# Optimization experiments

Hardware: AMD Instinct MI355X
Metric: run time of the kernel (lower is better)

## Reference

```python
import jax, jax.numpy as jnp
import numpy as np

BN_EPS = 1e-5


def gcn_conv(x, src, dst, n, W, b):
    # PyG GCNConv: h = x @ W; add self-loops; symmetric deg^{-1/2} norm; scatter-add; + bias
    h = x @ W
    sl = jnp.arange(n, dtype=src.dtype)
    src_f = jnp.concatenate([src, sl])
    dst_f = jnp.concatenate([dst, sl])
    deg = jax.ops.segment_sum(jnp.ones_like(dst_f, dtype=h.dtype), dst_f, num_segments=n)
    dis = jnp.where(deg > 0, jax.lax.rsqrt(jnp.maximum(deg, 1.0)), 0.0)
    norm = dis[src_f] * dis[dst_f]                       # [E+N]
    msg = h[src_f] * norm[:, None]                       # gather + scale
    out = jax.ops.segment_sum(msg, dst_f, num_segments=n)  # scatter-add
    return out + b


def batchnorm(x, g, b):
    # training-mode BatchNorm1d (batch statistics), deterministic
    mu = jnp.mean(x, axis=0)
    var = jnp.mean((x - mu) ** 2, axis=0)
    return g * (x - mu) * jax.lax.rsqrt(var + BN_EPS) + b


def setup_inputs() -> dict:
    key = jax.random.key(0)
    ks = jax.random.split(key, 12)
    N, E, F_IN, D, M, G = 40000, 640000, 128, 128, 256, 2000
    x = jax.random.normal(ks[0], (N, F_IN), dtype=jnp.float32)
    edge_index = jax.random.randint(ks[1], (2, E), 0, N, dtype=jnp.int64)
    batch = jnp.sort(jax.random.randint(ks[2], (N,), 0, G, dtype=jnp.int64))
    s = lambda fi: 1.0 / np.sqrt(fi)
    W1 = jax.random.normal(ks[3], (F_IN, D), dtype=jnp.float32) * s(F_IN)
    b1 = jnp.zeros((D,), jnp.float32)
    W2 = jax.random.normal(ks[4], (D, D), dtype=jnp.float32) * s(D)
    b2 = jnp.zeros((D,), jnp.float32)
    bn1_g = jnp.ones((D,), jnp.float32); bn1_b = jnp.zeros((D,), jnp.float32)
    bn2_g = jnp.ones((D,), jnp.float32); bn2_b = jnp.zeros((D,), jnp.float32)
    fc1_w = jax.random.normal(ks[5], (D, M), dtype=jnp.float32) * s(D)
    fc1_b = jnp.zeros((M,), jnp.float32)
    fc2_w = jax.random.normal(ks[6], (M, M), dtype=jnp.float32) * s(M)
    fc2_b = jnp.zeros((M,), jnp.float32)
    fc3_w = jax.random.normal(ks[7], (M, 1), dtype=jnp.float32) * s(M)
    fc3_b = jnp.zeros((1,), jnp.float32)
    return dict(x=x, edge_index=edge_index, batch=batch, num_graphs=G,
                W1=W1, b1=b1, W2=W2, b2=b2,
                bn1_g=bn1_g, bn1_b=bn1_b, bn2_g=bn2_g, bn2_b=bn2_b,
                fc1_w=fc1_w, fc1_b=fc1_b, fc2_w=fc2_w, fc2_b=fc2_b,
                fc3_w=fc3_w, fc3_b=fc3_b)


def reference(x, edge_index, batch, num_graphs, W1, b1, W2, b2,
              bn1_g, bn1_b, bn2_g, bn2_b,
              fc1_w, fc1_b, fc2_w, fc2_b, fc3_w, fc3_b):
    n = x.shape[0]
    src, dst = edge_index[0], edge_index[1]
    h = gcn_conv(x, src, dst, n, W1, b1)
    h = jax.nn.relu(batchnorm(h, bn1_g, bn1_b))
    h = gcn_conv(h, src, dst, n, W2, b2)
    h = jax.nn.relu(batchnorm(h, bn2_g, bn2_b))
    g = jax.ops.segment_sum(h, batch, num_segments=num_graphs)  # scatter_sum pooling [G, D]
    g = jax.nn.relu(g @ fc1_w + fc1_b)   # dropout is identity in eval
    g = jax.nn.relu(g @ fc2_w + fc2_b)
    return g @ fc3_w + fc3_b             # [G, 1]
```

## Files before the change

kernel.cpp:

```cpp
#include <hip/hip_runtime.h>

#define NN 40000
#define NE 640000
#define DF 128
#define NG 2000
#define NCH 157
#define FILLB 625
#define GEMM_BLKS 313

typedef unsigned int u32;
typedef __attribute__((ext_vector_type(8))) short short8;
typedef __attribute__((ext_vector_type(4))) float floatx4;

__device__ inline float2 bf2_to_f2(u32 u) {
    return make_float2(__uint_as_float(u << 16), __uint_as_float(u & 0xffff0000u));
}
__device__ inline u32 f_to_bf(float f) {
    u32 u = __float_as_uint(f);
    return (u + 0x7fffu + ((u >> 16) & 1u)) >> 16;
}
__device__ inline u32 pack_bf2(float a, float b) {
    return f_to_bf(a) | (f_to_bf(b) << 16);
}
__device__ inline float bf_to_f(short s) {
    return __uint_as_float(((u32)(unsigned short)s) << 16);
}

template<bool BF16IN, bool FUSE_BN, bool WT_F32>
__device__ __forceinline__ void gemm_core(const void* __restrict__ Xv, const void* __restrict__ wsrc,
                                          u32* __restrict__ outb, const float* __restrict__ slots,
                                          const float* __restrict__ gam, const float* __restrict__ bet, int bid) {
    __shared__ unsigned short uni[128 * 136];
    __shared__ float sc[128], sh[128];
    unsigned short* wlds = uni;
    unsigned short* clds = uni;
    int tid = threadIdx.x;
    int row0 = bid * 128;

    if (FUSE_BN) {
        if (tid < 128) {
            float s = 0.f, q = 0.f;
            for (int k = 0; k < 64; k++) {
                s += slots[k * 256 + tid];
                q += slots[k * 256 + 128 + tid];
            }
            const float inv_n = 1.0f / (float)NN;
            float mu = s * inv_n;
            float va = fmaf(-mu, mu, q * inv_n);
            float a = gam[tid] * rsqrtf(va + 1e-5f);
            sc[tid] = a;
            sh[tid] = fmaf(-mu, a, bet[tid]);
        }
    }
    if (WT_F32) {
        const float* W = (const float*)wsrc;
        for (int i = tid; i < 16384; i += 256) {
            int k = i >> 7, c = i & 127;
            wlds[c * 136 + k] = (unsigned short)f_to_bf(W[i]);
        }
    } else {
        const unsigned short* wt = (const unsigned short*)wsrc;
        for (int i = tid; i < 2048; i += 256) {
            int c = i >> 4, s = i & 15;
            *(uint4*)&wlds[c * 136 + s * 8] = ((const uint4*)wt)[i];
        }
    }
    __syncthreads();

    int lane = tid & 63;
    int wave = tid >> 6;
    int qr = lane >> 4;
    int rl = lane & 15;
    int rA0 = row0 + wave * 32 + rl;
    int rA1 = rA0 + 16;
    int rA0c = rA0 < NN ? rA0 : NN - 1;
    int rA1c = rA1 < NN ? rA1 : NN - 1;

    floatx4 acc[2][8];
#pragma unroll
    for (int a = 0; a < 2; a++)
#pragma unroll
        for (int b = 0; b < 8; b++) acc[a][b] = (floatx4){0.f, 0.f, 0.f, 0.f};

#pragma unroll
    for (int kb = 0; kb < 4; kb++) {
        int k0 = kb * 32 + qr * 8;
        short8 a0, a1;
        if (!BF16IN) {
            const float* p0 = (const float*)Xv + (size_t)rA0c * DF + k0;
            const float* p1 = (const float*)Xv + (size_t)rA1c * DF + k0;
            float4 u0 = *(const float4*)p0, u1 = *(const float4*)(p0 + 4);
            float4 v0 = *(const float4*)p1, v1 = *(const float4*)(p1 + 4);
            float fa[8] = {u0.x, u0.y, u0.z, u0.w, u1.x, u1.y, u1.z, u1.w};
            float fb[8] = {v0.x, v0.y, v0.z, v0.w, v1.x, v1.y, v1.z, v1.w};
#pragma unroll
            for (int j = 0; j < 8; j++) { a0[j] = (short)f_to_bf(fa[j]); a1[j] = (short)f_to_bf(fb[j]); }
        } else {
            a0 = *(const short8*)((const u32*)Xv + (size_t)rA0c * 64 + (k0 >> 1));
            a1 = *(const short8*)((const u32*)Xv + (size_t)rA1c * 64 + (k0 >> 1));
            if (FUSE_BN) {
                float4 s0 = *(const float4*)&sc[k0], s1 = *(const float4*)&sc[k0 + 4];
                float4 h0 = *(const float4*)&sh[k0], h1 = *(const float4*)&sh[k0 + 4];
                float ss[8] = {s0.x, s0.y, s0.z, s0.w, s1.x, s1.y, s1.z, s1.w};
                float hh[8] = {h0.x, h0.y, h0.z, h0.w, h1.x, h1.y, h1.z, h1.w};
#pragma unroll
                for (int j = 0; j < 8; j++) {
                    float f0 = fmaxf(fmaf(bf_to_f(a0[j]), ss[j], hh[j]), 0.f);
                    float f1 = fmaxf(fmaf(bf_to_f(a1[j]), ss[j], hh[j]), 0.f);
                    a0[j] = (short)f_to_bf(f0);
                    a1[j] = (short)f_to_bf(f1);
                }
            }
        }
#pragma unroll
        for (int ct = 0; ct < 8; ct++) {
            short8 bfr = *(const short8*)&wlds[(ct * 16 + rl) * 136 + k0];
            acc[0][ct] = __builtin_amdgcn_mfma_f32_16x16x32_bf16(a0, bfr, acc[0][ct], 0, 0, 0);
            acc[1][ct] = __builtin_amdgcn_mfma_f32_16x16x32_bf16(a1, bfr, acc[1][ct], 0, 0, 0);
        }
    }
    __syncthreads();
#pragma unroll
    for (int rt = 0; rt < 2; rt++)
#pragma unroll
        for (int ct = 0; ct < 8; ct++)
#pragma unroll
            for (int r = 0; r < 4; r++) {
                int lr = wave * 32 + rt * 16 + qr * 4 + r;
                int c = ct * 16 + rl;
                clds[lr * 136 + c] = (unsigned short)f_to_bf(acc[rt][ct][r]);
            }
    __syncthreads();
    for (int i = tid; i < 2048; i += 256) {
        int lr = i >> 4, s = i & 15;
        int grow = row0 + lr;
        if (grow < NN) {
            uint4 v = *(const uint4*)&clds[lr * 136 + s * 8];
            ((uint4*)(outb + (size_t)grow * 64))[s] = v;
        }
    }
}

__global__ __launch_bounds__(256, 4) void k_countgemm(const int* __restrict__ dst, int* __restrict__ deg,
                                                      int* __restrict__ rank,
                                                      const float* __restrict__ W1, const float* __restrict__ W2,
                                                      unsigned short* __restrict__ wt2,
                                                      const float* __restrict__ X, u32* __restrict__ outb) {
    int bid = blockIdx.x;
    if (bid < FILLB) {
        int e0 = bid * 1024 + threadIdx.x;
        int d0 = dst[e0], d1 = dst[e0 + 256], d2 = dst[e0 + 512], d3 = dst[e0 + 768];
        int r0 = atomicAdd(&deg[d0], 1);
        int r1 = atomicAdd(&deg[d1], 1);
        int r2 = atomicAdd(&deg[d2], 1);
        int r3 = atomicAdd(&deg[d3], 1);
        rank[e0] = r0;
        rank[e0 + 256] = r1;
        rank[e0 + 512] = r2;
        rank[e0 + 768] = r3;
        return;
    }
    if (bid == FILLB) {
        for (int i = threadIdx.x; i < 128 * 128; i += 256) {
            int k = i >> 7, c = i & 127;
            wt2[c * 128 + k] = (unsigned short)f_to_bf(W2[i]);
        }
        return;
    }
    gemm_core<false, false, true>(X, W1, outb, nullptr, nullptr, nullptr, bid - FILLB - 1);
}

__global__ __launch_bounds__(256) void k_scan(const int* __restrict__ deg,
                                              int* __restrict__ row_ptr, float* __restrict__ dis) {
    __shared__ int red[256];
    __shared__ int ls[256];
    int tid = threadIdx.x;
    int blk = blockIdx.x;
    int limit = blk * 256;
    int partial = 0;
    for (int i = tid; i < limit; i += 256) partial += deg[i];
    red[tid] = partial;
    int i = limit + tid;
    int d = (i < NN) ? deg[i] : 0;
    ls[tid] = d;
    __syncthreads();
#pragma unroll
    for (int off = 128; off > 0; off >>= 1) {
        if (tid < off) red[tid] += red[tid + off];
        __syncthreads();
    }
    int base = red[0];
#pragma unroll
    for (int off = 1; off < 256; off <<= 1) {
        int t = (tid >= off) ? ls[tid - off] : 0;
        __syncthreads();
        ls[tid] += t;
        __syncthreads();
    }
    if (i < NN) {
        int r = base + ls[tid] - d;
        row_ptr[i] = r;
        dis[i] = rsqrtf((float)(d + 1));
    }
    if (blk == NCH - 1 && tid == 0) row_ptr[NN] = NE;
}

__global__ __launch_bounds__(256) void k_fill(const int* __restrict__ src, const int* __restrict__ dst,
                                              const int* __restrict__ rank, const int* __restrict__ row_ptr,
                                              int* __restrict__ col) {
    int e0 = blockIdx.x * 1024 + threadIdx.x;
    int d0 = dst[e0], d1 = dst[e0 + 256], d2 = dst[e0 + 512], d3 = dst[e0 + 768];
    int s0 = src[e0], s1 = src[e0 + 256], s2 = src[e0 + 512], s3 = src[e0 + 768];
    int r0 = rank[e0], r1 = rank[e0 + 256], r2 = rank[e0 + 512], r3 = rank[e0 + 768];
    col[row_ptr[d0] + r0] = s0;
    col[row_ptr[d1] + r1] = s1;
    col[row_ptr[d2] + r2] = s2;
    col[row_ptr[d3] + r3] = s3;
}

__global__ __launch_bounds__(256, 4) void k_gemm2(const u32* __restrict__ Hb, const unsigned short* __restrict__ wt2,
                                                  u32* __restrict__ outb, const float* __restrict__ slots,
                                                  const float* __restrict__ gam, const float* __restrict__ bet) {
    gemm_core<true, true, false>(Hb, wt2, outb, slots, gam, bet, blockIdx.x);
}

__global__ __launch_bounds__(256) void k_gather(const u32* __restrict__ Hb, const int* __restrict__ row_ptr,
                                                const int* __restrict__ col, const float* __restrict__ dis,
                                                const float* __restrict__ bias, u32* __restrict__ outb,
                                                float* __restrict__ slots) {
    __shared__ float sred[4][128];
    __shared__ float qred[4][128];
    int t = threadIdx.x & 63;
    int wv = threadIdx.x >> 6;
    int node = blockIdx.x * 4 + wv;
    float di = dis[node];
    float2 acc;
    {
        float2 a = bf2_to_f2(Hb[(size_t)node * 64 + t]);
        float s = di * di;
        acc = make_float2(a.x * s, a.y * s);
    }
    int lo = row_ptr[node], hi = row_ptr[node + 1];
    for (int base = lo; base < hi; base += 64) {
        int m = hi - base; if (m > 64) m = 64;
        int sidx = 0; float sw = 0.f;
        if (t < m) { sidx = col[base + t]; sw = di * dis[sidx]; }
        int j = 0;
        for (; j + 8 <= m; j += 8) {
            int s0 = __shfl(sidx, j),     s1 = __shfl(sidx, j + 1);
            int s2 = __shfl(sidx, j + 2), s3 = __shfl(sidx, j + 3);
            int s4 = __shfl(sidx, j + 4), s5 = __shfl(sidx, j + 5);
            int s6 = __shfl(sidx, j + 6), s7 = __shfl(sidx, j + 7);
            float w0 = __shfl(sw, j),     w1 = __shfl(sw, j + 1);
            float w2 = __shfl(sw, j + 2), w3 = __shfl(sw, j + 3);
            float w4 = __shfl(sw, j + 4), w5 = __shfl(sw, j + 5);
            float w6 = __shfl(sw, j + 6), w7 = __shfl(sw, j + 7);
            u32 u0 = Hb[(size_t)s0 * 64 + t], u1 = Hb[(size_t)s1 * 64 + t];
            u32 u2 = Hb[(size_t)s2 * 64 + t], u3 = Hb[(size_t)s3 * 64 + t];
            u32 u4 = Hb[(size_t)s4 * 64 + t], u5 = Hb[(size_t)s5 * 64 + t];
            u32 u6 = Hb[(size_t)s6 * 64 + t], u7 = Hb[(size_t)s7 * 64 + t];
            float2 h0 = bf2_to_f2(u0), h1 = bf2_to_f2(u1), h2 = bf2_to_f2(u2), h3 = bf2_to_f2(u3);
            float2 h4 = bf2_to_f2(u4), h5 = bf2_to_f2(u5), h6 = bf2_to_f2(u6), h7 = bf2_to_f2(u7);
            acc.x = fmaf(h3.x, w3, fmaf(h2.x, w2, fmaf(h1.x, w1, fmaf(h0.x, w0, acc.x))));
            acc.y = fmaf(h3.y, w3, fmaf(h2.y, w2, fmaf(h1.y, w1, fmaf(h0.y, w0, acc.y))));
            acc.x = fmaf(h7.x, w7, fmaf(h6.x, w6, fmaf(h5.x, w5, fmaf(h4.x, w4, acc.x))));
            acc.y = fmaf(h7.y, w7, fmaf(h6.y, w6, fmaf(h5.y, w5, fmaf(h4.y, w4, acc.y))));
        }
        for (; j < m; j++) {
            int s0 = __shfl(sidx, j); float w0 = __shfl(sw, j);
            float2 h0 = bf2_to_f2(Hb[(size_t)s0 * 64 + t]);
            acc.x = fmaf(h0.x, w0, acc.x);
            acc.y = fmaf(h0.y, w0, acc.y);
        }
    }
    float2 b = ((const float2*)bias)[t];
    acc.x += b.x; acc.y += b.y;
    outb[(size_t)node * 64 + t] = pack_bf2(acc.x, acc.y);
    sred[wv][2 * t] = acc.x;     sred[wv][2 * t + 1] = acc.y;
    qred[wv][2 * t] = acc.x * acc.x; qred[wv][2 * t + 1] = acc.y * acc.y;
    __syncthreads();
    int tid = threadIdx.x;
    if (tid < 128) {
        float s = sred[0][tid] + sred[1][tid] + sred[2][tid] + sred[3][tid];
        float q = qred[0][tid] + qred[1][tid] + qred[2][tid] + qred[3][tid];
        int slot = blockIdx.x & 63;
        atomicAdd(&slots[slot * 256 + tid], s);
        atomicAdd(&slots[slot * 256 + 128 + tid], q);
    }
}

__global__ __launch_bounds__(256) void k_poolfc(const u32* __restrict__ Hb, const int* __restrict__ batch,
                                                const float* __restrict__ slots,
                                                const float* __restrict__ gam, const float* __restrict__ bet,
                                                const float* __restrict__ fc1w, const float* __restrict__ fc1b,
                                                const float* __restrict__ fc2w, const float* __restrict__ fc2b,
                                                const float* __restrict__ fc3w, const float* __restrict__ fc3b,
                                                float* __restrict__ out) {
    __shared__ float sc[128], sh[128];
    __shared__ float pooled[4][128];
    __shared__ float g1[4][256];
    __shared__ float g2[4][256];
    __shared__ int bnds[5];
    int tid = threadIdx.x;
    int gbase = blockIdx.x * 4;
    if (tid < 128) {
        float s = 0.f, q = 0.f;
        for (int k = 0; k < 64; k++) {
            s += slots[k * 256 + tid];
            q += slots[k * 256 + 128 + tid];
        }
        const float inv_n = 1.0f / (float)NN;
        float mu = s * inv_n;
        float va = fmaf(-mu, mu, q * inv_n);
        float a = gam[tid] * rsqrtf(va + 1e-5f);
        sc[tid] = a;
        sh[tid] = fmaf(-mu, a, bet[tid]);
    } else if (tid < 133) {
        int target = gbase + (tid - 128);
        int a = 0, b = NN;
        while (a < b) { int m = (a + b) >> 1; if (batch[m] < target) a = m + 1; else b = m; }
        bnds[tid - 128] = a;
    }
    __syncthreads();
    {
        int g = tid >> 6, p = tid & 63;
        int lo = bnds[g], hi = bnds[g + 1];
        float a0 = 0.f, a1 = 0.f;
        float sc0 = sc[2 * p], sh0 = sh[2 * p], sc1 = sc[2 * p + 1], sh1 = sh[2 * p + 1];
        for (int i = lo; i < hi; i++) {
            float2 v = bf2_to_f2(Hb[(size_t)i * 64 + p]);
            a0 += fmaxf(fmaf(v.x, sc0, sh0), 0.f);
            a1 += fmaxf(fmaf(v.y, sc1, sh1), 0.f);
        }
        pooled[g][2 * p] = a0;
        pooled[g][2 * p + 1] = a1;
    }
    __syncthreads();
    {
        float x0 = 0.f, x1 = 0.f, x2 = 0.f, x3 = 0.f;
        for (int k = 0; k < 128; k++) {
            float wv = fc1w[k * 256 + tid];
            x0 = fmaf(pooled[0][k], wv, x0);
            x1 = fmaf(pooled[1][k], wv, x1);
            x2 = fmaf(pooled[2][k], wv, x2);
            x3 = fmaf(pooled[3][k], wv, x3);
        }
        float bb = fc1b[tid];
        g1[0][tid] = fmaxf(x0 + bb, 0.f);
        g1[1][tid] = fmaxf(x1 + bb, 0.f);
        g1[2][tid] = fmaxf(x2 + bb, 0.f);
        g1[3][tid] = fmaxf(x3 + bb, 0.f);
    }
    __syncthreads();
    {
        float x0 = 0.f, x1 = 0.f, x2 = 0.f, x3 = 0.f;
        for (int k = 0; k < 256; k++) {
            float wv = fc2w[k * 256 + tid];
            x0 = fmaf(g1[0][k], wv, x0);
            x1 = fmaf(g1[1][k], wv, x1);
            x2 = fmaf(g1[2][k], wv, x2);
            x3 = fmaf(g1[3][k], wv, x3);
        }
        float bb = fc2b[tid];
        g2[0][tid] = fmaxf(x0 + bb, 0.f);
        g2[1][tid] = fmaxf(x1 + bb, 0.f);
        g2[2][tid] = fmaxf(x2 + bb, 0.f);
        g2[3][tid] = fmaxf(x3 + bb, 0.f);
    }
    __syncthreads();
    {
        int lane = tid & 63, wv = tid >> 6;
        float s = fmaf(g2[wv][lane], fc3w[lane],
                  fmaf(g2[wv][64 + lane], fc3w[64 + lane],
                  fmaf(g2[wv][128 + lane], fc3w[128 + lane],
                       g2[wv][192 + lane] * fc3w[192 + lane])));
        for (int off = 32; off > 0; off >>= 1) s += __shfl_down(s, off);
        if (lane == 0) out[gbase + wv] = s + fc3b[0];
    }
}

extern "C" void kernel_launch(void* const* d_in, const int* in_sizes, int n_in,
                              void* d_out, int out_size, void* d_ws, size_t ws_size,
                              hipStream_t stream) {
    const float* x    = (const float*)d_in[0];
    const int*   ei   = (const int*)d_in[1];
    const int*   batch= (const int*)d_in[2];
    const float* W1   = (const float*)d_in[4];
    const float* b1   = (const float*)d_in[5];
    const float* W2   = (const float*)d_in[6];
    const float* b2   = (const float*)d_in[7];
    const float* bn1g = (const float*)d_in[8];
    const float* bn1b = (const float*)d_in[9];
    const float* bn2g = (const float*)d_in[10];
    const float* bn2b = (const float*)d_in[11];
    const float* fc1w = (const float*)d_in[12];
    const float* fc1b = (const float*)d_in[13];
    const float* fc2w = (const float*)d_in[14];
    const float* fc2b = (const float*)d_in[15];
    const float* fc3w = (const float*)d_in[16];
    const float* fc3b = (const float*)d_in[17];
    const int* src = ei;
    const int* dst = ei + NE;
    float* outp = (float*)d_out;

    char* w = (char*)d_ws;
    size_t o = 0;
    auto alloc = [&](size_t bytes) -> char* {
        char* p = w + o;
        o = (o + bytes + 255) & ~(size_t)255;
        return p;
    };
    int*   deg     = (int*)alloc((size_t)NN * 4);
    float* slotsA  = (float*)alloc(64 * 256 * 4);
    float* slotsB  = (float*)alloc(64 * 256 * 4);
    char*  zend    = w + o;
    int*   row_ptr = (int*)alloc((size_t)(NN + 1) * 4);
    int*   rank    = (int*)alloc((size_t)NE * 4);
    int*   col     = (int*)alloc((size_t)NE * 4);
    float* dis     = (float*)alloc((size_t)NN * 4);
    unsigned short* wt2 = (unsigned short*)alloc(128 * 128 * 2);
    u32*   bufA    = (u32*)alloc((size_t)NN * 64 * 4);
    u32*   bufB    = (u32*)alloc((size_t)NN * 64 * 4);

    hipMemsetAsync(deg, 0, (size_t)(zend - (char*)deg), stream);

    k_countgemm<<<FILLB + 1 + GEMM_BLKS, 256, 0, stream>>>(dst, deg, rank, W1, W2, wt2, x, bufA);
    k_scan<<<NCH, 256, 0, stream>>>(deg, row_ptr, dis);
    k_fill<<<FILLB, 256, 0, stream>>>(src, dst, rank, row_ptr, col);
    k_gather<<<NN / 4, 256, 0, stream>>>(bufA, row_ptr, col, dis, b1, bufB, slotsA);
    k_gemm2<<<GEMM_BLKS, 256, 0, stream>>>(bufB, wt2, bufA, slotsA, bn1g, bn1b);
    k_gather<<<NN / 4, 256, 0, stream>>>(bufA, row_ptr, col, dis, b2, bufB, slotsB);
    k_poolfc<<<NG / 4, 256, 0, stream>>>(bufB, batch, slotsB, bn2g, bn2b,
                                         fc1w, fc1b, fc2w, fc2b, fc3w, fc3b, outp);
}
```

Measured before the change: 276.2 us.

## Build CSR with per-block LDS degree counting and fused scan-fill

Replaces the global-atomic degree count with 157 blocks that each scan the full dst array and count edges for their own 256-node window using shared-memory atomics. The scan and fill kernels are merged into one that keeps row pointers in LDS, and the memset is replaced by zeroing blocks inside the first kernel. This removes global atomic contention, one kernel launch and a memset. In exchange every block reads all 640K dst entries, about 157x redundant reads (mostly L2 hits), and rank and col writes become scattered.

```diff
diff --git a/kernel.cpp b/kernel.cpp
--- a/kernel.cpp
+++ b/kernel.cpp
@@ -5,7 +5,6 @@
 #define DF 128
 #define NG 2000
 #define NCH 157
-#define FILLB 625
 #define GEMM_BLKS 313
 
 typedef unsigned int u32;
@@ -142,45 +141,62 @@
 }
 
 __global__ __launch_bounds__(256, 4) void k_countgemm(const int* __restrict__ dst, int* __restrict__ deg,
-                                                      int* __restrict__ rank,
+                                                      int* __restrict__ rank, float* __restrict__ slots0,
                                                       const float* __restrict__ W1, const float* __restrict__ W2,
                                                       unsigned short* __restrict__ wt2,
                                                       const float* __restrict__ X, u32* __restrict__ outb) {
+    __shared__ int wdeg[256];
     int bid = blockIdx.x;
-    if (bid < FILLB) {
-        int e0 = bid * 1024 + threadIdx.x;
-        int d0 = dst[e0], d1 = dst[e0 + 256], d2 = dst[e0 + 512], d3 = dst[e0 + 768];
-        int r0 = atomicAdd(&deg[d0], 1);
-        int r1 = atomicAdd(&deg[d1], 1);
-        int r2 = atomicAdd(&deg[d2], 1);
-        int r3 = atomicAdd(&deg[d3], 1);
-        rank[e0] = r0;
-        rank[e0 + 256] = r1;
-        rank[e0 + 512] = r2;
-        rank[e0 + 768] = r3;
+    int tid = threadIdx.x;
+    if (bid < NCH) {
+        int lo = bid << 8;
+        wdeg[tid] = 0;
+        __syncthreads();
+        const int4* dst4 = (const int4*)dst;
+        for (int it = tid; it < NE / 4; it += 256) {
+            int4 d = dst4[it];
+            int e = it * 4;
+            int t0 = d.x - lo, t1 = d.y - lo, t2 = d.z - lo, t3 = d.w - lo;
+            if ((u32)t0 < 256u) rank[e]     = atomicAdd(&wdeg[t0], 1);
+            if ((u32)t1 < 256u) rank[e + 1] = atomicAdd(&wdeg[t1], 1);
+            if ((u32)t2 < 256u) rank[e + 2] = atomicAdd(&wdeg[t2], 1);
+            if ((u32)t3 < 256u) rank[e + 3] = atomicAdd(&wdeg[t3], 1);
+        }
+        __syncthreads();
+        int node = lo + tid;
+        if (node < NN) deg[node] = wdeg[tid];
         return;
     }
-    if (bid == FILLB) {
-        for (int i = threadIdx.x; i < 128 * 128; i += 256) {
+    if (bid < NCH + 2) {
+        float* s = slots0 + (bid - NCH) * 64 * 256;
+        for (int i = tid; i < 64 * 256; i += 256) s[i] = 0.f;
+        return;
+    }
+    if (bid == NCH + 2) {
+        for (int i = tid; i < 128 * 128; i += 256) {
             int k = i >> 7, c = i & 127;
             wt2[c * 128 + k] = (unsigned short)f_to_bf(W2[i]);
         }
         return;
     }
-    gemm_core<false, false, true>(X, W1, outb, nullptr, nullptr, nullptr, bid - FILLB - 1);
-}
-
-__global__ __launch_bounds__(256) void k_scan(const int* __restrict__ deg,
-                                              int* __restrict__ row_ptr, float* __restrict__ dis) {
+    gemm_core<false, false, true>(X, W1, outb, nullptr, nullptr, nullptr, bid - NCH - 3);
+}
+
+__global__ __launch_bounds__(256) void k_scanfill(const int* __restrict__ deg,
+                                                  const int* __restrict__ src, const int* __restrict__ dst,
+                                                  const int* __restrict__ rank,
+                                                  int* __restrict__ row_ptr, float* __restrict__ dis,
+                                                  int* __restrict__ col) {
     __shared__ int red[256];
     __shared__ int ls[256];
+    __shared__ int rowp[256];
     int tid = threadIdx.x;
     int blk = blockIdx.x;
-    int limit = blk * 256;
+    int lo = blk << 8;
     int partial = 0;
-    for (int i = tid; i < limit; i += 256) partial += deg[i];
+    for (int i = tid; i < lo; i += 256) partial += deg[i];
     red[tid] = partial;
-    int i = limit + tid;
+    int i = lo + tid;
     int d = (i < NN) ? deg[i] : 0;
     ls[tid] = d;
     __syncthreads();
@@ -197,25 +213,24 @@
         ls[tid] += t;
         __syncthreads();
     }
+    int r = base + ls[tid] - d;
+    rowp[tid] = r;
     if (i < NN) {
-        int r = base + ls[tid] - d;
         row_ptr[i] = r;
         dis[i] = rsqrtf((float)(d + 1));
     }
     if (blk == NCH - 1 && tid == 0) row_ptr[NN] = NE;
-}
-
-__global__ __launch_bounds__(256) void k_fill(const int* __restrict__ src, const int* __restrict__ dst,
-                                              const int* __restrict__ rank, const int* __restrict__ row_ptr,
-                                              int* __restrict__ col) {
-    int e0 = blockIdx.x * 1024 + threadIdx.x;
-    int d0 = dst[e0], d1 = dst[e0 + 256], d2 = dst[e0 + 512], d3 = dst[e0 + 768];
-    int s0 = src[e0], s1 = src[e0 + 256], s2 = src[e0 + 512], s3 = src[e0 + 768];
-    int r0 = rank[e0], r1 = rank[e0 + 256], r2 = rank[e0 + 512], r3 = rank[e0 + 768];
-    col[row_ptr[d0] + r0] = s0;
-    col[row_ptr[d1] + r1] = s1;
-    col[row_ptr[d2] + r2] = s2;
-    col[row_ptr[d3] + r3] = s3;
+    __syncthreads();
+    const int4* dst4 = (const int4*)dst;
+    for (int it = tid; it < NE / 4; it += 256) {
+        int4 dd = dst4[it];
+        int e = it * 4;
+        int t0 = dd.x - lo, t1 = dd.y - lo, t2 = dd.z - lo, t3 = dd.w - lo;
+        if ((u32)t0 < 256u) col[rowp[t0] + rank[e]]     = src[e];
+        if ((u32)t1 < 256u) col[rowp[t1] + rank[e + 1]] = src[e + 1];
+        if ((u32)t2 < 256u) col[rowp[t2] + rank[e + 2]] = src[e + 2];
+        if ((u32)t3 < 256u) col[rowp[t3] + rank[e + 3]] = src[e + 3];
+    }
 }
 
 __global__ __launch_bounds__(256, 4) void k_gemm2(const u32* __restrict__ Hb, const unsigned short* __restrict__ wt2,
@@ -411,9 +426,7 @@
         return p;
     };
     int*   deg     = (int*)alloc((size_t)NN * 4);
-    float* slotsA  = (float*)alloc(64 * 256 * 4);
-    float* slotsB  = (float*)alloc(64 * 256 * 4);
-    char*  zend    = w + o;
+    float* slots0  = (float*)alloc((size_t)2 * 64 * 256 * 4);
     int*   row_ptr = (int*)alloc((size_t)(NN + 1) * 4);
     int*   rank    = (int*)alloc((size_t)NE * 4);
     int*   col     = (int*)alloc((size_t)NE * 4);
@@ -421,12 +434,11 @@
     unsigned short* wt2 = (unsigned short*)alloc(128 * 128 * 2);
     u32*   bufA    = (u32*)alloc((size_t)NN * 64 * 4);
     u32*   bufB    = (u32*)alloc((size_t)NN * 64 * 4);
-
-    hipMemsetAsync(deg, 0, (size_t)(zend - (char*)deg), stream);
-
-    k_countgemm<<<FILLB + 1 + GEMM_BLKS, 256, 0, stream>>>(dst, deg, rank, W1, W2, wt2, x, bufA);
-    k_scan<<<NCH, 256, 0, stream>>>(deg, row_ptr, dis);
-    k_fill<<<FILLB, 256, 0, stream>>>(src, dst, rank, row_ptr, col);
+    float* slotsA  = slots0;
+    float* slotsB  = slots0 + 64 * 256;
+
+    k_countgemm<<<NCH + 3 + GEMM_BLKS, 256, 0, stream>>>(dst, deg, rank, slots0, W1, W2, wt2, x, bufA);
+    k_scanfill<<<NCH, 256, 0, stream>>>(deg, src, dst, rank, row_ptr, dis, col);
     k_gather<<<NN / 4, 256, 0, stream>>>(bufA, row_ptr, col, dis, b1, bufB, slotsA);
     k_gemm2<<<GEMM_BLKS, 256, 0, stream>>>(bufB, wt2, bufA, slotsA, bn1g, bn1b);
     k_gather<<<NN / 4, 256, 0, stream>>>(bufA, row_ptr, col, dis, b2, bufB, slotsB);
```

Result: slower. 752.6 us (+172.4%).

## Pack fp16 source norm into CSR column word and halve GEMM row tile

Applied to the files above, without the earlier changes.

The CSR fill kernel now stores each edge's source index in the low 16 bits and an fp16 copy of the source's deg^-1/2 in the high 16 bits. The gather kernel therefore decodes the edge weight from the column word instead of doing a dependent random load of dis[src] per edge. Separately, the GEMM tiles drop from 128 to 64 rows per block, doubling the block count to raise parallelism, with the row bound checks removed because 40000 divides evenly by 64. The trade-offs are fp16 precision on the normalisation factor and a hard limit of 65536 nodes from the 16-bit index.

```diff
diff --git a/kernel.cpp b/kernel.cpp
--- a/kernel.cpp
+++ b/kernel.cpp
@@ -1,4 +1,5 @@
 #include <hip/hip_runtime.h>
+#include <hip/hip_fp16.h>
 
 #define NN 40000
 #define NE 640000
@@ -6,7 +7,7 @@
 #define NG 2000
 #define NCH 157
 #define FILLB 625
-#define GEMM_BLKS 313
+#define GEMM_BLKS 625
 
 typedef unsigned int u32;
 typedef __attribute__((ext_vector_type(8))) short short8;
@@ -24,6 +25,9 @@
 }
 __device__ inline float bf_to_f(short s) {
     return __uint_as_float(((u32)(unsigned short)s) << 16);
+}
+__device__ inline float colw_to_f(int cw) {
+    return __half2float(__ushort_as_half((unsigned short)((u32)cw >> 16)));
 }
 
 template<bool BF16IN, bool FUSE_BN, bool WT_F32>
@@ -35,7 +39,7 @@
     unsigned short* wlds = uni;
     unsigned short* clds = uni;
     int tid = threadIdx.x;
-    int row0 = bid * 128;
+    int row0 = bid * 64;
 
     if (FUSE_BN) {
         if (tid < 128) {
@@ -71,33 +75,24 @@
     int wave = tid >> 6;
     int qr = lane >> 4;
     int rl = lane & 15;
-    int rA0 = row0 + wave * 32 + rl;
-    int rA1 = rA0 + 16;
-    int rA0c = rA0 < NN ? rA0 : NN - 1;
-    int rA1c = rA1 < NN ? rA1 : NN - 1;
-
-    floatx4 acc[2][8];
-#pragma unroll
-    for (int a = 0; a < 2; a++)
-#pragma unroll
-        for (int b = 0; b < 8; b++) acc[a][b] = (floatx4){0.f, 0.f, 0.f, 0.f};
+    int rA = row0 + wave * 16 + rl;
+
+    floatx4 acc[8];
+#pragma unroll
+    for (int b = 0; b < 8; b++) acc[b] = (floatx4){0.f, 0.f, 0.f, 0.f};
 
 #pragma unroll
     for (int kb = 0; kb < 4; kb++) {
         int k0 = kb * 32 + qr * 8;
-        short8 a0, a1;
+        short8 a0;
         if (!BF16IN) {
-            const float* p0 = (const float*)Xv + (size_t)rA0c * DF + k0;
-            const float* p1 = (const float*)Xv + (size_t)rA1c * DF + k0;
+            const float* p0 = (const float*)Xv + (size_t)rA * DF + k0;
             float4 u0 = *(const float4*)p0, u1 = *(const float4*)(p0 + 4);
-            float4 v0 = *(const float4*)p1, v1 = *(const float4*)(p1 + 4);
             float fa[8] = {u0.x, u0.y, u0.z, u0.w, u1.x, u1.y, u1.z, u1.w};
-            float fb[8] = {v0.x, v0.y, v0.z, v0.w, v1.x, v1.y, v1.z, v1.w};
-#pragma unroll
-            for (int j = 0; j < 8; j++) { a0[j] = (short)f_to_bf(fa[j]); a1[j] = (short)f_to_bf(fb[j]); }
+#pragma unroll
+            for (int j = 0; j < 8; j++) a0[j] = (short)f_to_bf(fa[j]);
         } else {
-            a0 = *(const short8*)((const u32*)Xv + (size_t)rA0c * 64 + (k0 >> 1));
-            a1 = *(const short8*)((const u32*)Xv + (size_t)rA1c * 64 + (k0 >> 1));
+            a0 = *(const short8*)((const u32*)Xv + (size_t)rA * 64 + (k0 >> 1));
             if (FUSE_BN) {
                 float4 s0 = *(const float4*)&sc[k0], s1 = *(const float4*)&sc[k0 + 4];
                 float4 h0 = *(const float4*)&sh[k0], h1 = *(const float4*)&sh[k0 + 4];
@@ -106,38 +101,30 @@
 #pragma unroll
                 for (int j = 0; j < 8; j++) {
                     float f0 = fmaxf(fmaf(bf_to_f(a0[j]), ss[j], hh[j]), 0.f);
-                    float f1 = fmaxf(fmaf(bf_to_f(a1[j]), ss[j], hh[j]), 0.f);
                     a0[j] = (short)f_to_bf(f0);
-                    a1[j] = (short)f_to_bf(f1);
                 }
             }
         }
 #pragma unroll
         for (int ct = 0; ct < 8; ct++) {
             short8 bfr = *(const short8*)&wlds[(ct * 16 + rl) * 136 + k0];
-            acc[0][ct] = __builtin_amdgcn_mfma_f32_16x16x32_bf16(a0, bfr, acc[0][ct], 0, 0, 0);
-            acc[1][ct] = __builtin_amdgcn_mfma_f32_16x16x32_bf16(a1, bfr, acc[1][ct], 0, 0, 0);
-        }
-    }
-    __syncthreads();
-#pragma unroll
-    for (int rt = 0; rt < 2; rt++)
-#pragma unroll
-        for (int ct = 0; ct < 8; ct++)
-#pragma unroll
-            for (int r = 0; r < 4; r++) {
-                int lr = wave * 32 + rt * 16 + qr * 4 + r;
-                int c = ct * 16 + rl;
-                clds[lr * 136 + c] = (unsigned short)f_to_bf(acc[rt][ct][r]);
-            }
-    __syncthreads();
-    for (int i = tid; i < 2048; i += 256) {
+            acc[ct] = __builtin_amdgcn_mfma_f32_16x16x32_bf16(a0, bfr, acc[ct], 0, 0, 0);
+        }
+    }
+    __syncthreads();
+#pragma unroll
+    for (int ct = 0; ct < 8; ct++)
+#pragma unroll
+        for (int r = 0; r < 4; r++) {
+            int lr = wave * 16 + qr * 4 + r;
+            int c = ct * 16 + rl;
+            clds[lr * 136 + c] = (unsigned short)f_to_bf(acc[ct][r]);
+        }
+    __syncthreads();
+    for (int i = tid; i < 1024; i += 256) {
         int lr = i >> 4, s = i & 15;
-        int grow = row0 + lr;
-        if (grow < NN) {
-            uint4 v = *(const uint4*)&clds[lr * 136 + s * 8];
-            ((uint4*)(outb + (size_t)grow * 64))[s] = v;
-        }
+        uint4 v = *(const uint4*)&clds[lr * 136 + s * 8];
+        ((uint4*)(outb + (size_t)(row0 + lr) * 64))[s] = v;
     }
 }
 
@@ -207,15 +194,19 @@
 
 __global__ __launch_bounds__(256) void k_fill(const int* __restrict__ src, const int* __restrict__ dst,
                                               const int* __restrict__ rank, const int* __restrict__ row_ptr,
-                                              int* __restrict__ col) {
+                                              const float* __restrict__ dis, u32* __restrict__ col) {
     int e0 = blockIdx.x * 1024 + threadIdx.x;
     int d0 = dst[e0], d1 = dst[e0 + 256], d2 = dst[e0 + 512], d3 = dst[e0 + 768];
     int s0 = src[e0], s1 = src[e0 + 256], s2 = src[e0 + 512], s3 = src[e0 + 768];
     int r0 = rank[e0], r1 = rank[e0 + 256], r2 = rank[e0 + 512], r3 = rank[e0 + 768];
-    col[row_ptr[d0] + r0] = s0;
-    col[row_ptr[d1] + r1] = s1;
-    col[row_ptr[d2] + r2] = s2;
-    col[row_ptr[d3] + r3] = s3;
+    u32 h0 = (u32)__half_as_ushort(__float2half(dis[s0]));
+    u32 h1 = (u32)__half_as_ushort(__float2half(dis[s1]));
+    u32 h2 = (u32)__half_as_ushort(__float2half(dis[s2]));
+    u32 h3 = (u32)__half_as_ushort(__float2half(dis[s3]));
+    col[row_ptr[d0] + r0] = (u32)s0 | (h0 << 16);
+    col[row_ptr[d1] + r1] = (u32)s1 | (h1 << 16);
+    col[row_ptr[d2] + r2] = (u32)s2 | (h2 << 16);
+    col[row_ptr[d3] + r3] = (u32)s3 | (h3 << 16);
 }
 
 __global__ __launch_bounds__(256, 4) void k_gemm2(const u32* __restrict__ Hb, const unsigned short* __restrict__ wt2,
@@ -225,7 +216,7 @@
 }
 
 __global__ __launch_bounds__(256) void k_gather(const u32* __restrict__ Hb, const int* __restrict__ row_ptr,
-                                                const int* __restrict__ col, const float* __restrict__ dis,
+                                                const u32* __restrict__ col, const float* __restrict__ dis,
                                                 const float* __restrict__ bias, u32* __restrict__ outb,
                                                 float* __restrict__ slots) {
     __shared__ float sred[4][128];
@@ -243,22 +234,22 @@
     int lo = row_ptr[node], hi = row_ptr[node + 1];
     for (int base = lo; base < hi; base += 64) {
         int m = hi - base; if (m > 64) m = 64;
-        int sidx = 0; float sw = 0.f;
-        if (t < m) { sidx = col[base + t]; sw = di * dis[sidx]; }
+        int cw = 0;
+        if (t < m) cw = (int)col[base + t];
         int j = 0;
         for (; j + 8 <= m; j += 8) {
-            int s0 = __shfl(sidx, j),     s1 = __shfl(sidx, j + 1);
-            int s2 = __shfl(sidx, j + 2), s3 = __shfl(sidx, j + 3);
-            int s4 = __shfl(sidx, j + 4), s5 = __shfl(sidx, j + 5);
-            int s6 = __shfl(sidx, j + 6), s7 = __shfl(sidx, j + 7);
-            float w0 = __shfl(sw, j),     w1 = __shfl(sw, j + 1);
-            float w2 = __shfl(sw, j + 2), w3 = __shfl(sw, j + 3);
-            float w4 = __shfl(sw, j + 4), w5 = __shfl(sw, j + 5);
-            float w6 = __shfl(sw, j + 6), w7 = __shfl(sw, j + 7);
-            u32 u0 = Hb[(size_t)s0 * 64 + t], u1 = Hb[(size_t)s1 * 64 + t];
-            u32 u2 = Hb[(size_t)s2 * 64 + t], u3 = Hb[(size_t)s3 * 64 + t];
-            u32 u4 = Hb[(size_t)s4 * 64 + t], u5 = Hb[(size_t)s5 * 64 + t];
-            u32 u6 = Hb[(size_t)s6 * 64 + t], u7 = Hb[(size_t)s7 * 64 + t];
+            int c0 = __shfl(cw, j),     c1 = __shfl(cw, j + 1);
+            int c2 = __shfl(cw, j + 2), c3 = __shfl(cw, j + 3);
+            int c4 = __shfl(cw, j + 4), c5 = __shfl(cw, j + 5);
+            int c6 = __shfl(cw, j + 6), c7 = __shfl(cw, j + 7);
+            u32 u0 = Hb[(size_t)(c0 & 0xffff) * 64 + t], u1 = Hb[(size_t)(c1 & 0xffff) * 64 + t];
+            u32 u2 = Hb[(size_t)(c2 & 0xffff) * 64 + t], u3 = Hb[(size_t)(c3 & 0xffff) * 64 + t];
+            u32 u4 = Hb[(size_t)(c4 & 0xffff) * 64 + t], u5 = Hb[(size_t)(c5 & 0xffff) * 64 + t];
+            u32 u6 = Hb[(size_t)(c6 & 0xffff) * 64 + t], u7 = Hb[(size_t)(c7 & 0xffff) * 64 + t];
+            float w0 = di * colw_to_f(c0), w1 = di * colw_to_f(c1);
+            float w2 = di * colw_to_f(c2), w3 = di * colw_to_f(c3);
+            float w4 = di * colw_to_f(c4), w5 = di * colw_to_f(c5);
+            float w6 = di * colw_to_f(c6), w7 = di * colw_to_f(c7);
             float2 h0 = bf2_to_f2(u0), h1 = bf2_to_f2(u1), h2 = bf2_to_f2(u2), h3 = bf2_to_f2(u3);
             float2 h4 = bf2_to_f2(u4), h5 = bf2_to_f2(u5), h6 = bf2_to_f2(u6), h7 = bf2_to_f2(u7);
             acc.x = fmaf(h3.x, w3, fmaf(h2.x, w2, fmaf(h1.x, w1, fmaf(h0.x, w0, acc.x))));
@@ -267,8 +258,9 @@
             acc.y = fmaf(h7.y, w7, fmaf(h6.y, w6, fmaf(h5.y, w5, fmaf(h4.y, w4, acc.y))));
         }
         for (; j < m; j++) {
-            int s0 = __shfl(sidx, j); float w0 = __shfl(sw, j);
-            float2 h0 = bf2_to_f2(Hb[(size_t)s0 * 64 + t]);
+            int c0 = __shfl(cw, j);
+            float w0 = di * colw_to_f(c0);
+            float2 h0 = bf2_to_f2(Hb[(size_t)(c0 & 0xffff) * 64 + t]);
             acc.x = fmaf(h0.x, w0, acc.x);
             acc.y = fmaf(h0.y, w0, acc.y);
         }
@@ -416,7 +408,7 @@
     char*  zend    = w + o;
     int*   row_ptr = (int*)alloc((size_t)(NN + 1) * 4);
     int*   rank    = (int*)alloc((size_t)NE * 4);
-    int*   col     = (int*)alloc((size_t)NE * 4);
+    u32*   col     = (u32*)alloc((size_t)NE * 4);
     float* dis     = (float*)alloc((size_t)NN * 4);
     unsigned short* wt2 = (unsigned short*)alloc(128 * 128 * 2);
     u32*   bufA    = (u32*)alloc((size_t)NN * 64 * 4);
@@ -426,7 +418,7 @@
 
     k_countgemm<<<FILLB + 1 + GEMM_BLKS, 256, 0, stream>>>(dst, deg, rank, W1, W2, wt2, x, bufA);
     k_scan<<<NCH, 256, 0, stream>>>(deg, row_ptr, dis);
-    k_fill<<<FILLB, 256, 0, stream>>>(src, dst, rank, row_ptr, col);
+    k_fill<<<FILLB, 256, 0, stream>>>(src, dst, rank, row_ptr, dis, col);
     k_gather<<<NN / 4, 256, 0, stream>>>(bufA, row_ptr, col, dis, b1, bufB, slotsA);
     k_gemm2<<<GEMM_BLKS, 256, 0, stream>>>(bufB, wt2, bufA, slotsA, bn1g, bn1b);
     k_gather<<<NN / 4, 256, 0, stream>>>(bufA, row_ptr, col, dis, b2, bufB, slotsB);
```

Measured after the change: 273.3 us. No clear change (-1.1%).
